# Kernel tuning notes

Measured on AMD Instinct MI355X. Metric: run time of the kernel, lower is better.

Reference implementation:

```python
import jax, jax.numpy as jnp
import numpy as np

N_EMB = 1024
HEAD_SIZE = 128


def setup_inputs() -> dict:
    key = jax.random.key(0)
    k1, k2, k3, k4 = jax.random.split(key, 4)
    B, T = 8, 4096
    x = jax.random.normal(k1, (B, T, N_EMB), dtype=jnp.float32)
    # nn.Linear(n_emb, head_size, bias=False) weights have shape [head_size, n_emb]
    s = 1.0 / np.sqrt(N_EMB)
    Wq = jax.random.uniform(k2, (HEAD_SIZE, N_EMB), jnp.float32, -s, s)
    Wk = jax.random.uniform(k3, (HEAD_SIZE, N_EMB), jnp.float32, -s, s)
    Wv = jax.random.uniform(k4, (HEAD_SIZE, N_EMB), jnp.float32, -s, s)
    return {"x": x, "Wq": Wq, "Wk": Wk, "Wv": Wv}


def reference(x, Wq, Wk, Wv):
    # x: [B, T, C]; W*: [H, C]
    B, T, C = x.shape
    H = Wq.shape[0]
    q = jnp.einsum('btc,hc->bth', x, Wq)
    k = jnp.einsum('btc,hc->bth', x, Wk)
    v = jnp.einsum('btc,hc->bth', x, Wv)
    scale = H ** -0.5
    wei = jnp.einsum('bth,bsh->bts', q, k) * scale  # [B, T, T]
    # causal mask: position t attends to s <= t
    causal = jnp.arange(T)[:, None] >= jnp.arange(T)[None, :]
    wei = jnp.where(causal, wei, -jnp.inf)
    wei = jax.nn.softmax(wei, axis=-1)
    # dropout treated as identity (eval mode)
    out = jnp.einsum('bts,bsh->bth', wei, v)  # [B, T, H]
    return out
```

## Files before the change

### kernel.cpp

```cpp
#include <hip/hip_runtime.h>
#include <hip/hip_bf16.h>

typedef __bf16 bf16_t;
typedef __attribute__((ext_vector_type(8))) __bf16 bf16x8;
typedef __attribute__((ext_vector_type(4))) __bf16 bf16x4;
typedef __attribute__((ext_vector_type(4))) float f32x4;

#define MFMA16(a, b, c) __builtin_amdgcn_mfma_f32_16x16x32_bf16((a), (b), (c), 0, 0, 0)

__device__ __forceinline__ void gload_lds16(const void* g, void* l) {
    __builtin_amdgcn_global_load_lds(
        (const __attribute__((address_space(1))) void*)g,
        (__attribute__((address_space(3))) void*)l, 16, 0, 0);
}

__global__ __launch_bounds__(256, 3) void proj_qkv(
    const float* __restrict__ X,
    const float* __restrict__ W0, const float* __restrict__ W1, const float* __restrict__ W2,
    bf16_t* __restrict__ O0, bf16_t* __restrict__ O1, bf16_t* __restrict__ O2)
{
    __shared__ __align__(16) char As[128 * 128];
    __shared__ __align__(16) char Bs[128 * 128];

    const int tid = threadIdx.x;
    const int wid = tid >> 6;
    const int lane = tid & 63;
    const int l15 = lane & 15, l4 = lane >> 4;
    const int wr = wid >> 1, wc = wid & 1;
    const int m0 = blockIdx.x * 128;

    const float* W = (blockIdx.y == 0) ? W0 : (blockIdx.y == 1 ? W1 : W2);

    const int r0 = tid >> 4;
    const int kq = tid & 15;
    const int swz = ((r0 & 7) << 4);

    f32x4 acc[4][4] = {};
    float4 xr[8];

    #pragma unroll
    for (int i = 0; i < 8; ++i)
        xr[i] = *(const float4*)(X + (size_t)(m0 + r0 + i * 16) * 1024 + kq * 4);

    for (int ks = 0; ks < 16; ++ks) {
        const int kb = ks * 64;
        #pragma unroll
        for (int i = 0; i < 8; ++i) {
            const int r = r0 + i * 16;
            bf16x4 av; av[0] = (bf16_t)xr[i].x; av[1] = (bf16_t)xr[i].y;
            av[2] = (bf16_t)xr[i].z; av[3] = (bf16_t)xr[i].w;
            *(bf16x4*)(As + r * 128 + ((kq * 8) ^ swz)) = av;
        }
        #pragma unroll
        for (int i = 0; i < 8; ++i) {
            const int r = r0 + i * 16;
            float4 wa = *(const float4*)(W + (size_t)r * 1024 + kb + kq * 4);
            bf16x4 wv; wv[0] = (bf16_t)wa.x; wv[1] = (bf16_t)wa.y;
            wv[2] = (bf16_t)wa.z; wv[3] = (bf16_t)wa.w;
            *(bf16x4*)(Bs + r * 128 + ((kq * 8) ^ swz)) = wv;
        }
        __syncthreads();
        if (ks < 15) {
            #pragma unroll
            for (int i = 0; i < 8; ++i)
                xr[i] = *(const float4*)(X + (size_t)(m0 + r0 + i * 16) * 1024 + kb + 64 + kq * 4);
        }
        #pragma unroll
        for (int kk = 0; kk < 64; kk += 32) {
            const int kbyte = 2 * kk + 16 * l4;
            bf16x8 af[4], bfr[4];
            #pragma unroll
            for (int mi = 0; mi < 4; ++mi) {
                int r = wr * 64 + mi * 16 + l15;
                af[mi] = *(const bf16x8*)(As + r * 128 + (kbyte ^ ((r & 7) << 4)));
            }
            #pragma unroll
            for (int ni = 0; ni < 4; ++ni) {
                int r = wc * 64 + ni * 16 + l15;
                bfr[ni] = *(const bf16x8*)(Bs + r * 128 + (kbyte ^ ((r & 7) << 4)));
            }
            #pragma unroll
            for (int mi = 0; mi < 4; ++mi)
                #pragma unroll
                for (int ni = 0; ni < 4; ++ni)
                    acc[mi][ni] = MFMA16(af[mi], bfr[ni], acc[mi][ni]);
        }
        __syncthreads();
    }

    if (blockIdx.y < 2) {
        const float sc = (blockIdx.y == 0) ? 0.12751754816f : 1.0f;
        bf16_t* O = (blockIdx.y == 0) ? O0 : O1;
        #pragma unroll
        for (int mi = 0; mi < 4; ++mi)
            #pragma unroll
            for (int ni = 0; ni < 4; ++ni) {
                int row = m0 + wr * 64 + mi * 16 + l4 * 4;
                int col = wc * 64 + ni * 16 + l15;
                #pragma unroll
                for (int r = 0; r < 4; ++r)
                    O[(size_t)(row + r) * 128 + col] = (bf16_t)(acc[mi][ni][r] * sc);
            }
    } else {
        #pragma unroll
        for (int mi = 0; mi < 4; ++mi)
            #pragma unroll
            for (int ni = 0; ni < 4; ++ni) {
                int row0 = m0 + wr * 64 + mi * 16 + l4 * 4;
                int col = wc * 64 + ni * 16 + l15;
                int bb = row0 >> 12, t0 = row0 & 4095;
                bf16x4 pk;
                #pragma unroll
                for (int r = 0; r < 4; ++r) pk[r] = (bf16_t)acc[mi][ni][r];
                *(bf16x4*)(O2 + ((size_t)bb << 19) + (size_t)col * 4096 + t0) = pk;
            }
    }
}

__global__ __launch_bounds__(256, 2) void attn_fwd(
    const bf16_t* __restrict__ Qb, const bf16_t* __restrict__ Kb,
    const bf16_t* __restrict__ Vtg, float* __restrict__ out, int Bn)
{
    __shared__ __align__(16) char lds[73728];

    const int tid = threadIdx.x, wid = tid >> 6, lane = tid & 63;
    const int l15 = lane & 15, l4 = lane >> 4;

    const int blk = blockIdx.x;
    const int b = blk % Bn;
    const int j = blk / Bn;

    const size_t base = (size_t)b * 4096 * 128;
    const size_t baseVT = (size_t)b << 19;

    char* Vw = lds + wid * 16384;
    char* Pw = lds + 65536 + wid * 2048;
    const int pswz = (l15 >> 1) & 3;
    const int vswz = (l15 >> 1) & 3;

    const int sh = lane >> 2;
    const int skb = (((lane & 3) ^ ((sh >> 1) & 3))) * 8;

    bf16x8 aones;
    #pragma unroll
    for (int e = 0; e < 8; ++e) aones[e] = (bf16_t)1.0f;

    for (int seg = 0; seg < 2; ++seg) {
        const int p = seg ? (127 - j) : j;
        const int q0 = p << 5;
        const int nt = (p >= wid) ? ((p - wid) >> 2) + 1 : 0;

        bf16x8 aq[2][4];
        #pragma unroll
        for (int qs = 0; qs < 2; ++qs)
            #pragma unroll
            for (int kf = 0; kf < 4; ++kf)
                aq[qs][kf] = *(const bf16x8*)(Qb + base
                    + (size_t)(q0 + 16 * qs + l15) * 128 + 32 * kf + 8 * l4);

        float mx[2] = {-1e30f, -1e30f};
        f32x4 ls_acc[2] = {};
        f32x4 o[2][8] = {};
        bf16x8 kreg[2][4];

        auto stageV = [&](int i) {
            const int kv0 = (wid + 4 * i) << 5;
            char* dst = Vw + (i & 1) * 8192;
            #pragma unroll
            for (int c = 0; c < 8; ++c) {
                const bf16_t* src = Vtg + baseVT + (size_t)(16 * c + sh) * 4096 + kv0 + skb;
                gload_lds16(src, dst + c * 1024);
            }
        };
        auto loadK = [&](int i) {
            const int kv0 = (wid + 4 * i) << 5;
            const bf16_t* kp = Kb + base + (size_t)(kv0 + l15) * 128 + 8 * l4;
            #pragma unroll
            for (int ni = 0; ni < 2; ++ni)
                #pragma unroll
                for (int kf = 0; kf < 4; ++kf)
                    kreg[ni][kf] = *(const bf16x8*)(kp + (size_t)ni * 2048 + kf * 32);
        };

        if (nt > 0) { loadK(0); stageV(0); }

        for (int i = 0; i < nt; ++i) {
            const int lt = wid + 4 * i;
            const int kv0 = lt << 5;

            f32x4 sa[2][2];
            #pragma unroll
            for (int qs = 0; qs < 2; ++qs)
                #pragma unroll
                for (int ni = 0; ni < 2; ++ni) sa[qs][ni] = (f32x4){0.f, 0.f, 0.f, 0.f};
            __builtin_amdgcn_s_setprio(1);
            #pragma unroll
            for (int kf = 0; kf < 4; ++kf)
                #pragma unroll
                for (int ni = 0; ni < 2; ++ni) {
                    sa[0][ni] = MFMA16(kreg[ni][kf], aq[0][kf], sa[0][ni]);
                    sa[1][ni] = MFMA16(kreg[ni][kf], aq[1][kf], sa[1][ni]);
                }
            __builtin_amdgcn_s_setprio(0);

            if (i + 1 < nt) loadK(i + 1);

            if (lt == p) {
                #pragma unroll
                for (int qs = 0; qs < 2; ++qs) {
                    const int qg = q0 + 16 * qs + l15;
                    #pragma unroll
                    for (int ni = 0; ni < 2; ++ni)
                        #pragma unroll
                        for (int r = 0; r < 4; ++r)
                            if (kv0 + 16 * ni + 4 * l4 + r > qg) sa[qs][ni][r] = -1e30f;
                }
            }

            #pragma unroll
            for (int qs = 0; qs < 2; ++qs) {
                float tm = fmaxf(fmaxf(fmaxf(sa[qs][0][0], sa[qs][0][1]),
                                       fmaxf(sa[qs][0][2], sa[qs][0][3])),
                                 fmaxf(fmaxf(sa[qs][1][0], sa[qs][1][1]),
                                       fmaxf(sa[qs][1][2], sa[qs][1][3])));
                if (__any(tm > mx[qs] + 8.0f)) {
                    tm = fmaxf(tm, __shfl_xor(tm, 16, 64));
                    tm = fmaxf(tm, __shfl_xor(tm, 32, 64));
                    const float mnew = fmaxf(mx[qs], tm);
                    const float c = exp2f(mx[qs] - mnew);
                    f32x4 lt4 = ls_acc[qs];
                    lt4[0] *= c; lt4[1] *= c; lt4[2] *= c; lt4[3] *= c;
                    ls_acc[qs] = lt4;
                    #pragma unroll
                    for (int mf = 0; mf < 8; ++mf) {
                        f32x4 t = o[qs][mf];
                        t[0] *= c; t[1] *= c; t[2] *= c; t[3] *= c;
                        o[qs][mf] = t;
                    }
                    mx[qs] = mnew;
                }
                #pragma unroll
                for (int ni = 0; ni < 2; ++ni) {
                    bf16x4 pv;
                    #pragma unroll
                    for (int r = 0; r < 4; ++r)
                        pv[r] = (bf16_t)exp2f(sa[qs][ni][r] - mx[qs]);
                    *(bf16x4*)(Pw + (16 * qs + l15) * 64
                               + (((2 * ni + (l4 >> 1)) ^ pswz) << 4) + 8 * (l4 & 1)) = pv;
                }
            }

            __builtin_amdgcn_sched_barrier(0);
            asm volatile("s_waitcnt vmcnt(8)" ::: "memory");
            __builtin_amdgcn_sched_barrier(0);

            char* Vbuf = Vw + (i & 1) * 8192;
            bf16x8 pa0 = *(const bf16x8*)(Pw + l15 * 64 + ((l4 ^ pswz) << 4));
            bf16x8 pa1 = *(const bf16x8*)(Pw + (16 + l15) * 64 + ((l4 ^ pswz) << 4));
            __builtin_amdgcn_s_setprio(1);
            ls_acc[0] = MFMA16(aones, pa0, ls_acc[0]);
            ls_acc[1] = MFMA16(aones, pa1, ls_acc[1]);
            #pragma unroll
            for (int mf = 0; mf < 8; ++mf) {
                bf16x8 av = *(const bf16x8*)(Vbuf + (16 * mf + l15) * 64
                                             + ((l4 ^ vswz) << 4));
                o[0][mf] = MFMA16(av, pa0, o[0][mf]);
                o[1][mf] = MFMA16(av, pa1, o[1][mf]);
            }
            __builtin_amdgcn_s_setprio(0);

            if (i + 1 < nt) stageV(i + 1);
        }

        asm volatile("s_waitcnt vmcnt(0)" ::: "memory");
        __syncthreads();
        #pragma unroll
        for (int qs = 0; qs < 2; ++qs)
            #pragma unroll
            for (int mf = 0; mf < 8; ++mf)
                *(f32x4*)(lds + wid * 16384 + (qs * 8 + mf) * 1024 + lane * 16) = o[qs][mf];
        if (l4 == 0) {
            #pragma unroll
            for (int qs = 0; qs < 2; ++qs)
                *(float2*)(lds + 65536 + wid * 256 + (qs * 16 + l15) * 8)
                    = make_float2(mx[qs], ls_acc[qs][0]);
        }
        __syncthreads();
        #pragma unroll
        for (int qs = 0; qs < 2; ++qs) {
            float mw[4], lw[4];
            #pragma unroll
            for (int w = 0; w < 4; ++w) {
                float2 st = *(const float2*)(lds + 65536 + w * 256 + (qs * 16 + l15) * 8);
                mw[w] = st.x; lw[w] = st.y;
            }
            const float M = fmaxf(fmaxf(mw[0], mw[1]), fmaxf(mw[2], mw[3]));
            float cw[4], L = 0.f;
            #pragma unroll
            for (int w = 0; w < 4; ++w) { cw[w] = exp2f(mw[w] - M); L += lw[w] * cw[w]; }
            const float inv = 1.f / L;
            #pragma unroll
            for (int mm = 0; mm < 2; ++mm) {
                const int mf = 2 * wid + mm;
                f32x4 acc = (f32x4){0.f, 0.f, 0.f, 0.f};
                #pragma unroll
                for (int w = 0; w < 4; ++w) {
                    f32x4 v = *(const f32x4*)(lds + w * 16384 + (qs * 8 + mf) * 1024 + lane * 16);
                    #pragma unroll
                    for (int e = 0; e < 4; ++e) acc[e] += v[e] * cw[w];
                }
                #pragma unroll
                for (int e = 0; e < 4; ++e) acc[e] *= inv;
                float* op = out + ((size_t)b * 4096 + q0 + 16 * qs + l15) * 128 + 16 * mf + 4 * l4;
                *(f32x4*)op = acc;
            }
        }
        __syncthreads();
    }
}

extern "C" void kernel_launch(void* const* d_in, const int* in_sizes, int n_in,
                              void* d_out, int out_size, void* d_ws, size_t ws_size,
                              hipStream_t stream) {
    const float* X  = (const float*)d_in[0];
    const float* Wq = (const float*)d_in[1];
    const float* Wk = (const float*)d_in[2];
    const float* Wv = (const float*)d_in[3];
    float* out = (float*)d_out;

    const int M = in_sizes[0] / 1024;
    const int Bn = M / 4096;

    bf16_t* Qb  = (bf16_t*)d_ws;
    bf16_t* KbP = Qb + (size_t)M * 128;
    bf16_t* VtP = KbP + (size_t)M * 128;

    proj_qkv<<<dim3(M / 128, 3), 256, 0, stream>>>(X, Wq, Wk, Wv, Qb, KbP, VtP);
    attn_fwd<<<dim3(64 * Bn), 256, 0, stream>>>(Qb, KbP, VtP, out, Bn);
}
```

Measured before the change: 137.4 us.

## Load V directly into registers and shrink LDS to raise attention occupancy

The attention kernel no longer stages V tiles into a double-buffered LDS region with async global-to-LDS loads. Each wave now reads its V fragments straight from global memory into registers, in two batches of four, just before the PV MFMAs. The epilogue cross-wave reduction is done one query sub-tile at a time so it can reuse a smaller LDS buffer. Together these cut shared memory from 72KB to 40KB and the launch bound moves from 2 to 3 blocks per CU, aiming for more resident waves to hide latency. The cost is that V loads are no longer prefetched a tile ahead, so their global latency sits in the critical path, and the higher occupancy target may pressure registers.

```diff
diff --git a/kernel.cpp b/kernel.cpp
--- a/kernel.cpp
+++ b/kernel.cpp
@@ -7,12 +7,6 @@
 typedef __attribute__((ext_vector_type(4))) float f32x4;
 
 #define MFMA16(a, b, c) __builtin_amdgcn_mfma_f32_16x16x32_bf16((a), (b), (c), 0, 0, 0)
-
-__device__ __forceinline__ void gload_lds16(const void* g, void* l) {
-    __builtin_amdgcn_global_load_lds(
-        (const __attribute__((address_space(1))) void*)g,
-        (__attribute__((address_space(3))) void*)l, 16, 0, 0);
-}
 
 __global__ __launch_bounds__(256, 3) void proj_qkv(
     const float* __restrict__ X,
@@ -117,11 +111,11 @@
     }
 }
 
-__global__ __launch_bounds__(256, 2) void attn_fwd(
+__global__ __launch_bounds__(256, 3) void attn_fwd(
     const bf16_t* __restrict__ Qb, const bf16_t* __restrict__ Kb,
     const bf16_t* __restrict__ Vtg, float* __restrict__ out, int Bn)
 {
-    __shared__ __align__(16) char lds[73728];
+    __shared__ __align__(16) char lds[40960];
 
     const int tid = threadIdx.x, wid = tid >> 6, lane = tid & 63;
     const int l15 = lane & 15, l4 = lane >> 4;
@@ -133,13 +127,8 @@
     const size_t base = (size_t)b * 4096 * 128;
     const size_t baseVT = (size_t)b << 19;
 
-    char* Vw = lds + wid * 16384;
-    char* Pw = lds + 65536 + wid * 2048;
+    char* Pw = lds + wid * 2048;
     const int pswz = (l15 >> 1) & 3;
-    const int vswz = (l15 >> 1) & 3;
-
-    const int sh = lane >> 2;
-    const int skb = (((lane & 3) ^ ((sh >> 1) & 3))) * 8;
 
     bf16x8 aones;
     #pragma unroll
@@ -163,15 +152,6 @@
         f32x4 o[2][8] = {};
         bf16x8 kreg[2][4];
 
-        auto stageV = [&](int i) {
-            const int kv0 = (wid + 4 * i) << 5;
-            char* dst = Vw + (i & 1) * 8192;
-            #pragma unroll
-            for (int c = 0; c < 8; ++c) {
-                const bf16_t* src = Vtg + baseVT + (size_t)(16 * c + sh) * 4096 + kv0 + skb;
-                gload_lds16(src, dst + c * 1024);
-            }
-        };
         auto loadK = [&](int i) {
             const int kv0 = (wid + 4 * i) << 5;
             const bf16_t* kp = Kb + base + (size_t)(kv0 + l15) * 128 + 8 * l4;
@@ -182,7 +162,7 @@
                     kreg[ni][kf] = *(const bf16x8*)(kp + (size_t)ni * 2048 + kf * 32);
         };
 
-        if (nt > 0) { loadK(0); stageV(0); }
+        if (nt > 0) loadK(0);
 
         for (int i = 0; i < nt; ++i) {
             const int lt = wid + 4 * i;
@@ -250,48 +230,41 @@
                 }
             }
 
-            __builtin_amdgcn_sched_barrier(0);
-            asm volatile("s_waitcnt vmcnt(8)" ::: "memory");
-            __builtin_amdgcn_sched_barrier(0);
-
-            char* Vbuf = Vw + (i & 1) * 8192;
             bf16x8 pa0 = *(const bf16x8*)(Pw + l15 * 64 + ((l4 ^ pswz) << 4));
             bf16x8 pa1 = *(const bf16x8*)(Pw + (16 + l15) * 64 + ((l4 ^ pswz) << 4));
-            __builtin_amdgcn_s_setprio(1);
             ls_acc[0] = MFMA16(aones, pa0, ls_acc[0]);
             ls_acc[1] = MFMA16(aones, pa1, ls_acc[1]);
-            #pragma unroll
-            for (int mf = 0; mf < 8; ++mf) {
-                bf16x8 av = *(const bf16x8*)(Vbuf + (16 * mf + l15) * 64
-                                             + ((l4 ^ vswz) << 4));
-                o[0][mf] = MFMA16(av, pa0, o[0][mf]);
-                o[1][mf] = MFMA16(av, pa1, o[1][mf]);
-            }
-            __builtin_amdgcn_s_setprio(0);
-
-            if (i + 1 < nt) stageV(i + 1);
-        }
-
-        asm volatile("s_waitcnt vmcnt(0)" ::: "memory");
-        __syncthreads();
-        #pragma unroll
-        for (int qs = 0; qs < 2; ++qs)
+            const bf16_t* vp = Vtg + baseVT + (size_t)l15 * 4096 + kv0 + 8 * l4;
+            #pragma unroll
+            for (int hf = 0; hf < 2; ++hf) {
+                bf16x8 av[4];
+                #pragma unroll
+                for (int m = 0; m < 4; ++m)
+                    av[m] = *(const bf16x8*)(vp + (size_t)(16 * (4 * hf + m)) * 4096);
+                __builtin_amdgcn_s_setprio(1);
+                #pragma unroll
+                for (int m = 0; m < 4; ++m) {
+                    o[0][4 * hf + m] = MFMA16(av[m], pa0, o[0][4 * hf + m]);
+                    o[1][4 * hf + m] = MFMA16(av[m], pa1, o[1][4 * hf + m]);
+                }
+                __builtin_amdgcn_s_setprio(0);
+            }
+        }
+
+        #pragma unroll
+        for (int qs = 0; qs < 2; ++qs) {
+            __syncthreads();
             #pragma unroll
             for (int mf = 0; mf < 8; ++mf)
-                *(f32x4*)(lds + wid * 16384 + (qs * 8 + mf) * 1024 + lane * 16) = o[qs][mf];
-        if (l4 == 0) {
-            #pragma unroll
-            for (int qs = 0; qs < 2; ++qs)
-                *(float2*)(lds + 65536 + wid * 256 + (qs * 16 + l15) * 8)
+                *(f32x4*)(lds + 8192 + wid * 8192 + mf * 1024 + lane * 16) = o[qs][mf];
+            if (l4 == 0)
+                *(float2*)(lds + wid * 256 + l15 * 8)
                     = make_float2(mx[qs], ls_acc[qs][0]);
-        }
-        __syncthreads();
-        #pragma unroll
-        for (int qs = 0; qs < 2; ++qs) {
+            __syncthreads();
             float mw[4], lw[4];
             #pragma unroll
             for (int w = 0; w < 4; ++w) {
-                float2 st = *(const float2*)(lds + 65536 + w * 256 + (qs * 16 + l15) * 8);
+                float2 st = *(const float2*)(lds + w * 256 + l15 * 8);
                 mw[w] = st.x; lw[w] = st.y;
             }
             const float M = fmaxf(fmaxf(mw[0], mw[1]), fmaxf(mw[2], mw[3]));
@@ -305,7 +278,7 @@
                 f32x4 acc = (f32x4){0.f, 0.f, 0.f, 0.f};
                 #pragma unroll
                 for (int w = 0; w < 4; ++w) {
-                    f32x4 v = *(const f32x4*)(lds + w * 16384 + (qs * 8 + mf) * 1024 + lane * 16);
+                    f32x4 v = *(const f32x4*)(lds + 8192 + w * 8192 + mf * 1024 + lane * 16);
                     #pragma unroll
                     for (int e = 0; e < 4; ++e) acc[e] += v[e] * cw[w];
                 }
```

Result: slower. 210.0 us (+52.8%).

## Single-buffer V tiles in LDS to fit three attention blocks per CU

Applied to the files above, without the earlier changes.

Cuts attention-kernel LDS from 72KB to 40KB by dropping the V double buffer and running the cross-wave output reduction one query sub-tile at a time. Launch bounds go to 3 blocks per CU. V fragments are now read into registers before the MFMAs, and an lgkmcnt wait is inserted before the next V prefetch so the single buffer is not overwritten while still being read. This trades prefetch overlap and extra register pressure for higher occupancy.

```diff
diff --git a/kernel.cpp b/kernel.cpp
--- a/kernel.cpp
+++ b/kernel.cpp
@@ -117,11 +117,11 @@
     }
 }
 
-__global__ __launch_bounds__(256, 2) void attn_fwd(
+__global__ __launch_bounds__(256, 3) void attn_fwd(
     const bf16_t* __restrict__ Qb, const bf16_t* __restrict__ Kb,
     const bf16_t* __restrict__ Vtg, float* __restrict__ out, int Bn)
 {
-    __shared__ __align__(16) char lds[73728];
+    __shared__ __align__(16) char lds[40960];
 
     const int tid = threadIdx.x, wid = tid >> 6, lane = tid & 63;
     const int l15 = lane & 15, l4 = lane >> 4;
@@ -133,8 +133,8 @@
     const size_t base = (size_t)b * 4096 * 128;
     const size_t baseVT = (size_t)b << 19;
 
-    char* Vw = lds + wid * 16384;
-    char* Pw = lds + 65536 + wid * 2048;
+    char* Vw = lds + wid * 8192;
+    char* Pw = lds + 32768 + wid * 2048;
     const int pswz = (l15 >> 1) & 3;
     const int vswz = (l15 >> 1) & 3;
 
@@ -165,11 +165,10 @@
 
         auto stageV = [&](int i) {
             const int kv0 = (wid + 4 * i) << 5;
-            char* dst = Vw + (i & 1) * 8192;
             #pragma unroll
             for (int c = 0; c < 8; ++c) {
                 const bf16_t* src = Vtg + baseVT + (size_t)(16 * c + sh) * 4096 + kv0 + skb;
-                gload_lds16(src, dst + c * 1024);
+                gload_lds16(src, Vw + c * 1024);
             }
         };
         auto loadK = [&](int i) {
@@ -254,44 +253,45 @@
             asm volatile("s_waitcnt vmcnt(8)" ::: "memory");
             __builtin_amdgcn_sched_barrier(0);
 
-            char* Vbuf = Vw + (i & 1) * 8192;
             bf16x8 pa0 = *(const bf16x8*)(Pw + l15 * 64 + ((l4 ^ pswz) << 4));
             bf16x8 pa1 = *(const bf16x8*)(Pw + (16 + l15) * 64 + ((l4 ^ pswz) << 4));
+            bf16x8 av[8];
+            #pragma unroll
+            for (int mf = 0; mf < 8; ++mf)
+                av[mf] = *(const bf16x8*)(Vw + (16 * mf + l15) * 64 + ((l4 ^ vswz) << 4));
             __builtin_amdgcn_s_setprio(1);
             ls_acc[0] = MFMA16(aones, pa0, ls_acc[0]);
             ls_acc[1] = MFMA16(aones, pa1, ls_acc[1]);
             #pragma unroll
             for (int mf = 0; mf < 8; ++mf) {
-                bf16x8 av = *(const bf16x8*)(Vbuf + (16 * mf + l15) * 64
-                                             + ((l4 ^ vswz) << 4));
-                o[0][mf] = MFMA16(av, pa0, o[0][mf]);
-                o[1][mf] = MFMA16(av, pa1, o[1][mf]);
+                o[0][mf] = MFMA16(av[mf], pa0, o[0][mf]);
+                o[1][mf] = MFMA16(av[mf], pa1, o[1][mf]);
             }
             __builtin_amdgcn_s_setprio(0);
 
-            if (i + 1 < nt) stageV(i + 1);
+            if (i + 1 < nt) {
+                __builtin_amdgcn_sched_barrier(0);
+                asm volatile("s_waitcnt lgkmcnt(0)" ::: "memory");
+                __builtin_amdgcn_sched_barrier(0);
+                stageV(i + 1);
+            }
         }
 
         asm volatile("s_waitcnt vmcnt(0)" ::: "memory");
-        __syncthreads();
-        #pragma unroll
-        for (int qs = 0; qs < 2; ++qs)
+        #pragma unroll
+        for (int qs = 0; qs < 2; ++qs) {
+            __syncthreads();
             #pragma unroll
             for (int mf = 0; mf < 8; ++mf)
-                *(f32x4*)(lds + wid * 16384 + (qs * 8 + mf) * 1024 + lane * 16) = o[qs][mf];
-        if (l4 == 0) {
-            #pragma unroll
-            for (int qs = 0; qs < 2; ++qs)
-                *(float2*)(lds + 65536 + wid * 256 + (qs * 16 + l15) * 8)
+                *(f32x4*)(lds + wid * 8192 + mf * 1024 + lane * 16) = o[qs][mf];
+            if (l4 == 0)
+                *(float2*)(lds + 32768 + wid * 256 + l15 * 8)
                     = make_float2(mx[qs], ls_acc[qs][0]);
-        }
-        __syncthreads();
-        #pragma unroll
-        for (int qs = 0; qs < 2; ++qs) {
+            __syncthreads();
             float mw[4], lw[4];
             #pragma unroll
             for (int w = 0; w < 4; ++w) {
-                float2 st = *(const float2*)(lds + 65536 + w * 256 + (qs * 16 + l15) * 8);
+                float2 st = *(const float2*)(lds + 32768 + w * 256 + l15 * 8);
                 mw[w] = st.x; lw[w] = st.y;
             }
             const float M = fmaxf(fmaxf(mw[0], mw[1]), fmaxf(mw[2], mw[3]));
@@ -305,7 +305,7 @@
                 f32x4 acc = (f32x4){0.f, 0.f, 0.f, 0.f};
                 #pragma unroll
                 for (int w = 0; w < 4; ++w) {
-                    f32x4 v = *(const f32x4*)(lds + w * 16384 + (qs * 8 + mf) * 1024 + lane * 16);
+                    f32x4 v = *(const f32x4*)(lds + w * 8192 + mf * 1024 + lane * 16);
                     #pragma unroll
                     for (int e = 0; e < 4; ++e) acc[e] += v[e] * cw[w];
                 }
```

New measurement: 302.1 us. 2.2x slower.
